# Kernel optimization log

Hardware: AMD Instinct MI355X
Metric: run time of the kernel (lower is better)

The kernel has to match this reference:

```python
import jax, jax.numpy as jnp
import numpy as np

MARGIN = 0.5
EPS = 1e-12  # matches torch F.normalize eps


def setup_inputs() -> dict:
    key = jax.random.key(0)
    embeddings = jax.random.normal(key, (8192, 256), dtype=jnp.float32)
    return {"embeddings": embeddings}


def reference(embeddings):
    n = embeddings.shape[0]
    # L2-normalize rows (torch F.normalize: x / max(||x||, eps))
    norm = jnp.linalg.norm(embeddings, axis=1, keepdims=True)
    e = embeddings / jnp.maximum(norm, EPS)
    sim = e @ e.T  # [n, n]
    # strict upper triangle mask (i < j)
    iu = jnp.triu(jnp.ones((n, n), dtype=bool), k=1)
    loss_sum = jnp.sum(jnp.where(iu, jax.nn.relu(sim - MARGIN), 0.0))
    count = n * (n - 1) // 2
    return loss_sum / count
```

## Files before the change

kernel.cpp:

```cpp
#include <hip/hip_runtime.h>
#include <hip/hip_fp16.h>

typedef __attribute__((ext_vector_type(4))) float f32x4;

#define NROWS 8192
#define DCOLS 256
#define MARGIN 0.5f
#define NT 64
#define NBLOCKS 544

__global__ __launch_bounds__(256) void norm_kernel(const float* __restrict__ x,
                                                   unsigned char* __restrict__ e) {
    const int t = threadIdx.x;
    const int l = t & 63;
    const int c = l & 31;
    const int row = blockIdx.x * 8 + (t >> 6) * 2 + (l >> 5);

    const float4 v0 = *reinterpret_cast<const float4*>(&x[row * DCOLS + c * 8]);
    const float4 v1 = *reinterpret_cast<const float4*>(&x[row * DCOLS + c * 8 + 4]);
    float ss = v0.x * v0.x + v0.y * v0.y + v0.z * v0.z + v0.w * v0.w
             + v1.x * v1.x + v1.y * v1.y + v1.z * v1.z + v1.w * v1.w;
#pragma unroll
    for (int off = 16; off >= 1; off >>= 1) ss += __shfl_xor(ss, off, 32);
    const float inv = 1.0f / fmaxf(sqrtf(ss), 1e-12f);

    const float f[8] = {v0.x, v0.y, v0.z, v0.w, v1.x, v1.y, v1.z, v1.w};
    unsigned int lo = 0, hi = 0;
#pragma unroll
    for (int i = 0; i < 4; ++i) {
        const unsigned short hb = __half_as_ushort(__float2half(f[i] * inv));
        lo |= (unsigned int)(hb >> 8) << (8 * i);
    }
#pragma unroll
    for (int i = 0; i < 4; ++i) {
        const unsigned short hb = __half_as_ushort(__float2half(f[4 + i] * inv));
        hi |= (unsigned int)(hb >> 8) << (8 * i);
    }
    uint2 o; o.x = lo; o.y = hi;
    *reinterpret_cast<uint2*>(e + (size_t)row * DCOLS + c * 8) = o;
}

__global__ __launch_bounds__(256, 3) void tile_kernel(const unsigned char* __restrict__ e,
                                                      float* __restrict__ part) {
    const int orig = blockIdx.x;
    int bb = (orig & 7) * 68 + (orig >> 3);
    int bi = 0;
    while (bb >= ((NT - bi) + 3) >> 2) { bb -= ((NT - bi) + 3) >> 2; ++bi; }
    const int j0 = bi + bb * 4;
    const int nj = min(4, NT - j0);
    const int NS = nj * 8;

    __shared__ char As[32768];
    __shared__ char Bw[4][4][1024];
    __shared__ float red[4];

    const int t = threadIdx.x;
    const int l = t & 63;
    const int w = t >> 6;
    const int wn = w;
    const int lr = l & 15;
    const int hk = l >> 4;
    const unsigned char* eA = e + (size_t)bi * 128 * DCOLS;
    const unsigned char* eB = e + (size_t)j0 * 128 * DCOLS + wn * 32 * DCOLS;
    char* myB = Bw[w][0];

#pragma unroll
    for (int i = 0; i < 8; ++i) {
        const int u = i * 256 + t;
        const int kt = u >> 8, khalf = (u >> 7) & 1, row = u & 127;
        __builtin_amdgcn_global_load_lds(
            (const __attribute__((address_space(1))) void*)(eA + row * DCOLS + kt * 32 + khalf * 16),
            (__attribute__((address_space(3))) void*)(As + u * 16), 16, 0, 0);
    }
#pragma unroll
    for (int p = 0; p < 3; ++p) {
        __builtin_amdgcn_global_load_lds(
            (const __attribute__((address_space(1))) void*)(eB + (l & 31) * DCOLS + p * 32 + (l >> 5) * 16),
            (__attribute__((address_space(3))) void*)(myB + p * 1024 + l * 16), 16, 0, 0);
    }
    asm volatile("s_waitcnt vmcnt(3)" ::: "memory");
    __builtin_amdgcn_s_barrier();
    __builtin_amdgcn_sched_barrier(0);

    const int rd_base = (hk >> 1) ? 1 : 0;
    const int aoff = rd_base * 2048 + lr * 16 + (hk & 1) * 8;
    const int boff = rd_base * 512 + lr * 16 + (hk & 1) * 8;

    f32x4 acc[8][2];
#pragma unroll
    for (int m = 0; m < 8; ++m)
#pragma unroll
        for (int n = 0; n < 2; ++n)
            acc[m][n] = (f32x4){0.f, 0.f, 0.f, 0.f};

    long afb[2][8], bfb[2][2];
    asm volatile("s_waitcnt vmcnt(2)" ::: "memory");
#pragma unroll
    for (int m = 0; m < 8; ++m)
        afb[0][m] = *reinterpret_cast<const long*>(As + 0 * 4096 + m * 256 + aoff);
#pragma unroll
    for (int n = 0; n < 2; ++n)
        bfb[0][n] = *reinterpret_cast<const long*>(myB + 0 * 1024 + n * 256 + boff);

    float local = 0.0f;
    for (int jx = 0; jx < nj; ++jx) {
        const int jt = j0 + jx;
#pragma unroll
        for (int kt = 0; kt < 8; ++kt) {
            const int s = jx * 8 + kt;
            const int cur = kt & 1, nxt = cur ^ 1;
            {
                int s3 = s + 3; if (s3 >= NS) s3 -= NS;
                __builtin_amdgcn_global_load_lds(
                    (const __attribute__((address_space(1))) void*)(eB
                        + (size_t)(s3 >> 3) * 128 * DCOLS
                        + (l & 31) * DCOLS + (s3 & 7) * 32 + (l >> 5) * 16),
                    (__attribute__((address_space(3))) void*)(myB + ((kt + 3) & 3) * 1024 + l * 16),
                    16, 0, 0);
            }
            const bool have_next = (kt < 7) || (jx + 1 < nj);
            if (have_next) {
                asm volatile("s_waitcnt vmcnt(2)" ::: "memory");
#pragma unroll
                for (int n = 0; n < 2; ++n)
                    bfb[nxt][n] = *reinterpret_cast<const long*>(
                        myB + ((kt + 1) & 3) * 1024 + n * 256 + boff);
#pragma unroll
                for (int m = 0; m < 8; ++m)
                    afb[nxt][m] = *reinterpret_cast<const long*>(
                        As + ((kt + 1) & 7) * 4096 + m * 256 + aoff);
            }
            __builtin_amdgcn_s_setprio(1);
#pragma unroll
            for (int m = 0; m < 8; ++m)
#pragma unroll
                for (int n = 0; n < 2; ++n)
                    acc[m][n] = __builtin_amdgcn_mfma_f32_16x16x32_bf8_bf8(
                        afb[cur][m], bfb[cur][n], acc[m][n], 0, 0, 0);
            __builtin_amdgcn_s_setprio(0);
        }
        const int gi0 = bi * 128;
        const int gj0 = jt * 128 + wn * 32;
        if (jt == bi) {
#pragma unroll
            for (int m = 0; m < 8; ++m)
#pragma unroll
                for (int n = 0; n < 2; ++n) {
#pragma unroll
                    for (int r = 0; r < 4; ++r) {
                        const int gi = gi0 + m * 16 + hk * 4 + r;
                        const int gj = gj0 + n * 16 + lr;
                        local += (gi < gj) ? fmaxf(acc[m][n][r] - MARGIN, 0.0f) : 0.0f;
                    }
                    acc[m][n] = (f32x4){0.f, 0.f, 0.f, 0.f};
                }
        } else {
#pragma unroll
            for (int m = 0; m < 8; ++m)
#pragma unroll
                for (int n = 0; n < 2; ++n) {
#pragma unroll
                    for (int r = 0; r < 4; ++r)
                        local += fmaxf(acc[m][n][r] - MARGIN, 0.0f);
                    acc[m][n] = (f32x4){0.f, 0.f, 0.f, 0.f};
                }
        }
    }

#pragma unroll
    for (int off = 32; off >= 1; off >>= 1) local += __shfl_down(local, off);
    if (l == 0) red[w] = local;
    __syncthreads();
    if (t == 0) part[orig] = red[0] + red[1] + red[2] + red[3];
}

__global__ __launch_bounds__(256) void fin_kernel(const float* __restrict__ part,
                                                  float* __restrict__ out) {
    __shared__ float red[4];
    const int t = threadIdx.x;
    float v = part[t] + part[t + 256] + (t < NBLOCKS - 512 ? part[t + 512] : 0.0f);
#pragma unroll
    for (int off = 32; off >= 1; off >>= 1) v += __shfl_down(v, off);
    if ((t & 63) == 0) red[t >> 6] = v;
    __syncthreads();
    if (t == 0) out[0] = (red[0] + red[1] + red[2] + red[3]) / 33550336.0f;
}

extern "C" void kernel_launch(void* const* d_in, const int* in_sizes, int n_in,
                              void* d_out, int out_size, void* d_ws, size_t ws_size,
                              hipStream_t stream) {
    const float* x = (const float*)d_in[0];
    float* out = (float*)d_out;
    unsigned char* e = (unsigned char*)d_ws;
    float* part = (float*)((char*)d_ws + (size_t)NROWS * DCOLS);

    norm_kernel<<<NROWS / 8, 256, 0, stream>>>(x, e);
    tile_kernel<<<NBLOCKS, 256, 0, stream>>>(e, part);
    fin_kernel<<<1, 256, 0, stream>>>(part, out);
}
```

Measured before the change: 33.28 us.

## Fuse final reduction into tile kernel via atomics and last-block completion

Removes the separate finalize kernel launch. Each tile block atomically adds its partial sum to a global accumulator, and the last block to increment a counter writes the normalized result. The accumulator and counter are reset inside the norm kernel. The s_setprio around the MFMA loop is also dropped. In exchange the float atomic summation order is nondeterministic, and there is a small cost from 544 contended atomics.

Measured after the change: 37.64 us. 13.1% more time.

```diff
diff --git a/kernel.cpp b/kernel.cpp
--- a/kernel.cpp
+++ b/kernel.cpp
@@ -10,7 +10,10 @@
 #define NBLOCKS 544
 
 __global__ __launch_bounds__(256) void norm_kernel(const float* __restrict__ x,
-                                                   unsigned char* __restrict__ e) {
+                                                   unsigned char* __restrict__ e,
+                                                   float* __restrict__ acc,
+                                                   unsigned int* __restrict__ cnt) {
+    if (blockIdx.x == 0 && threadIdx.x == 0) { acc[0] = 0.0f; cnt[0] = 0u; }
     const int t = threadIdx.x;
     const int l = t & 63;
     const int c = l & 31;
@@ -41,7 +44,9 @@
 }
 
 __global__ __launch_bounds__(256, 3) void tile_kernel(const unsigned char* __restrict__ e,
-                                                      float* __restrict__ part) {
+                                                      float* __restrict__ acc,
+                                                      unsigned int* __restrict__ cnt,
+                                                      float* __restrict__ out) {
     const int orig = blockIdx.x;
     int bb = (orig & 7) * 68 + (orig >> 3);
     int bi = 0;
@@ -86,12 +91,12 @@
     const int aoff = rd_base * 2048 + lr * 16 + (hk & 1) * 8;
     const int boff = rd_base * 512 + lr * 16 + (hk & 1) * 8;
 
-    f32x4 acc[8][2];
+    f32x4 acc_r[8][2];
 #pragma unroll
     for (int m = 0; m < 8; ++m)
 #pragma unroll
         for (int n = 0; n < 2; ++n)
-            acc[m][n] = (f32x4){0.f, 0.f, 0.f, 0.f};
+            acc_r[m][n] = (f32x4){0.f, 0.f, 0.f, 0.f};
 
     long afb[2][8], bfb[2][2];
     asm volatile("s_waitcnt vmcnt(2)" ::: "memory");
@@ -130,14 +135,12 @@
                     afb[nxt][m] = *reinterpret_cast<const long*>(
                         As + ((kt + 1) & 7) * 4096 + m * 256 + aoff);
             }
-            __builtin_amdgcn_s_setprio(1);
 #pragma unroll
             for (int m = 0; m < 8; ++m)
 #pragma unroll
                 for (int n = 0; n < 2; ++n)
-                    acc[m][n] = __builtin_amdgcn_mfma_f32_16x16x32_bf8_bf8(
-                        afb[cur][m], bfb[cur][n], acc[m][n], 0, 0, 0);
-            __builtin_amdgcn_s_setprio(0);
+                    acc_r[m][n] = __builtin_amdgcn_mfma_f32_16x16x32_bf8_bf8(
+                        afb[cur][m], bfb[cur][n], acc_r[m][n], 0, 0, 0);
         }
         const int gi0 = bi * 128;
         const int gj0 = jt * 128 + wn * 32;
@@ -150,9 +153,9 @@
                     for (int r = 0; r < 4; ++r) {
                         const int gi = gi0 + m * 16 + hk * 4 + r;
                         const int gj = gj0 + n * 16 + lr;
-                        local += (gi < gj) ? fmaxf(acc[m][n][r] - MARGIN, 0.0f) : 0.0f;
+                        local += (gi < gj) ? fmaxf(acc_r[m][n][r] - MARGIN, 0.0f) : 0.0f;
                     }
-                    acc[m][n] = (f32x4){0.f, 0.f, 0.f, 0.f};
+                    acc_r[m][n] = (f32x4){0.f, 0.f, 0.f, 0.f};
                 }
         } else {
 #pragma unroll
@@ -161,8 +164,8 @@
                 for (int n = 0; n < 2; ++n) {
 #pragma unroll
                     for (int r = 0; r < 4; ++r)
-                        local += fmaxf(acc[m][n][r] - MARGIN, 0.0f);
-                    acc[m][n] = (f32x4){0.f, 0.f, 0.f, 0.f};
+                        local += fmaxf(acc_r[m][n][r] - MARGIN, 0.0f);
+                    acc_r[m][n] = (f32x4){0.f, 0.f, 0.f, 0.f};
                 }
         }
     }
@@ -171,19 +174,16 @@
     for (int off = 32; off >= 1; off >>= 1) local += __shfl_down(local, off);
     if (l == 0) red[w] = local;
     __syncthreads();
-    if (t == 0) part[orig] = red[0] + red[1] + red[2] + red[3];
-}
-
-__global__ __launch_bounds__(256) void fin_kernel(const float* __restrict__ part,
-                                                  float* __restrict__ out) {
-    __shared__ float red[4];
-    const int t = threadIdx.x;
-    float v = part[t] + part[t + 256] + (t < NBLOCKS - 512 ? part[t + 512] : 0.0f);
-#pragma unroll
-    for (int off = 32; off >= 1; off >>= 1) v += __shfl_down(v, off);
-    if ((t & 63) == 0) red[t >> 6] = v;
-    __syncthreads();
-    if (t == 0) out[0] = (red[0] + red[1] + red[2] + red[3]) / 33550336.0f;
+    if (t == 0) {
+        atomicAdd(acc, red[0] + red[1] + red[2] + red[3]);
+        __threadfence();
+        const unsigned int old = atomicAdd(cnt, 1u);
+        if (old == NBLOCKS - 1) {
+            __threadfence();
+            const float s = atomicAdd(acc, 0.0f);
+            out[0] = s / 33550336.0f;
+        }
+    }
 }
 
 extern "C" void kernel_launch(void* const* d_in, const int* in_sizes, int n_in,
@@ -192,9 +192,9 @@
     const float* x = (const float*)d_in[0];
     float* out = (float*)d_out;
     unsigned char* e = (unsigned char*)d_ws;
-    float* part = (float*)((char*)d_ws + (size_t)NROWS * DCOLS);
-
-    norm_kernel<<<NROWS / 8, 256, 0, stream>>>(x, e);
-    tile_kernel<<<NBLOCKS, 256, 0, stream>>>(e, part);
-    fin_kernel<<<1, 256, 0, stream>>>(part, out);
+    float* acc = (float*)((char*)d_ws + (size_t)NROWS * DCOLS);
+    unsigned int* cnt = (unsigned int*)((char*)d_ws + (size_t)NROWS * DCOLS + 64);
+
+    norm_kernel<<<NROWS / 8, 256, 0, stream>>>(x, e, acc, cnt);
+    tile_kernel<<<NBLOCKS, 256, 0, stream>>>(e, acc, cnt, out);
 }
```
